# Performance work log

Measured on AMD Instinct MI355X. Metric: run time of the kernel, lower is better.

Reference implementation:

```python
import jax, jax.numpy as jnp
import numpy as np

TRIANGLE_TABLE = np.array([
    [-1, -1, -1, -1, -1, -1], [1, 0, 2, -1, -1, -1], [4, 0, 3, -1, -1, -1], [1, 4, 2, 1, 3, 4],
    [3, 1, 5, -1, -1, -1], [2, 3, 0, 2, 5, 3], [1, 4, 0, 1, 5, 4], [4, 2, 5, -1, -1, -1],
    [4, 5, 2, -1, -1, -1], [4, 1, 0, 4, 5, 1], [3, 2, 0, 3, 5, 2], [1, 3, 5, -1, -1, -1],
    [4, 1, 2, 4, 3, 1], [3, 0, 4, -1, -1, -1], [2, 0, 1, -1, -1, -1], [-1, -1, -1, -1, -1, -1]], np.int32)
NUM_TRIANGLES_TABLE = np.array([0, 1, 1, 2, 1, 2, 2, 1, 1, 2, 2, 1, 2, 1, 1, 0], np.int32)
BASE_TET_EDGES = np.array([0, 1, 0, 2, 0, 3, 1, 2, 1, 3, 2, 3], np.int32)


def _make_tet_grid(R):
    # Regular grid in [0,1]^3, each cube split into 6 tets along the 0-7 diagonal.
    r1 = R + 1
    gi, gj, gk = np.meshgrid(np.arange(r1), np.arange(r1), np.arange(r1), indexing='ij')
    verts = (np.stack([gi, gj, gk], -1).reshape(-1, 3) / R).astype(np.float32)  # (Nv,3)
    ci, cj, ck = np.meshgrid(np.arange(R), np.arange(R), np.arange(R), indexing='ij')
    ci, cj, ck = ci.ravel(), cj.ravel(), ck.ravel()
    def vid(dx, dy, dz):
        return ((ci + dx) * r1 + (cj + dy)) * r1 + (ck + dz)
    corners = [vid((c >> 2) & 1, (c >> 1) & 1, c & 1) for c in range(8)]
    tet_corners = [(0, 1, 3, 7), (0, 3, 2, 7), (0, 2, 6, 7), (0, 6, 4, 7), (0, 4, 5, 7), (0, 5, 1, 7)]
    tets = np.stack([np.stack([corners[a] for a in t], -1) for t in tet_corners], 1).reshape(-1, 4)
    return verts, tets.astype(np.int32)


def setup_inputs() -> dict:
    R = 64
    verts, tets = _make_tet_grid(R)
    key = jax.random.key(0)
    k1, k2 = jax.random.split(key)
    level = jax.random.normal(k1, (verts.shape[0],), dtype=jnp.float32)
    deformation = jax.random.normal(k2, (verts.shape[0], 3), dtype=jnp.float32)
    return {
        'level': level,
        'deformation': deformation,
        'grid_vertices': jnp.asarray(verts),
        'tet_indices': jnp.asarray(tets),
        'resolution': R,
    }


def reference(level, deformation, grid_vertices, tet_indices, resolution):
    # normalize_grid_deformation: (range_hi - range_lo)/res * tanh(offsets), range = (0,1)
    pos = grid_vertices + jnp.tanh(deformation) / resolution  # (Nv,3)
    occ = level > 0                                           # (Nv,)
    occ_f = occ[tet_indices]                                  # (F,4)
    occ_sum = occ_f.sum(-1)
    valid = (occ_sum > 0) & (occ_sum < 4)
    vt = tet_indices[valid]                                   # (Fv,4)
    occ_valid = occ_f[valid]                                  # (Fv,4)
    # per-tet edges, each sorted (min,max) -> dedup
    edges = vt[:, jnp.asarray(BASE_TET_EDGES)].reshape(-1, 2)  # (6*Fv,2)
    edges = jnp.sort(edges, axis=1)
    unique_edges, idx_map = jnp.unique(edges, axis=0, return_inverse=True)
    idx_map = idx_map.reshape(-1)
    # edges that actually cross the isosurface (exactly one endpoint inside)
    mask_edges = occ[unique_edges].sum(-1) == 1               # (U,)
    mapping = jnp.where(mask_edges, jnp.cumsum(mask_edges.astype(jnp.int32)) - 1, -1)
    idx_map = mapping[idx_map].reshape(-1, 6)                 # (Fv,6)
    interp_v = unique_edges[mask_edges]                       # (M,2)
    # linear interpolation of crossing point along each edge
    ep = pos[interp_v]                                        # (M,2,3)
    es = level[interp_v] * jnp.array([1.0, -1.0], dtype=level.dtype)  # (M,2) = [sdf0, -sdf1]
    w = es[:, ::-1] / es.sum(1, keepdims=True)                # (M,2) = [-sdf1, sdf0]/(sdf0-sdf1)
    verts_out = (ep * w[:, :, None]).sum(1)                   # (M,3)
    # triangle table lookup
    v_id = jnp.array([1, 2, 4, 8], dtype=jnp.int32)
    tetindex = (occ_valid.astype(jnp.int32) * v_id).sum(-1)   # (Fv,)
    tri_tab = jnp.asarray(TRIANGLE_TABLE)
    num_tri = jnp.asarray(NUM_TRIANGLES_TABLE)[tetindex]
    m1 = num_tri == 1
    m2 = num_tri == 2
    f1 = jnp.take_along_axis(idx_map[m1], tri_tab[tetindex[m1]][:, :3], axis=1).reshape(-1, 3)
    f2 = jnp.take_along_axis(idx_map[m2], tri_tab[tetindex[m2]][:, :6], axis=1).reshape(-1, 3)
    faces = jnp.concatenate([f1, f2], axis=0)                 # (Nf,3)
    return verts_out, faces
```

## Files before the change

### kernel.cpp

```cpp
#include <hip/hip_runtime.h>
#include <math.h>


typedef unsigned long long ull;

#define ST_LD(p)    __hip_atomic_load((p), __ATOMIC_RELAXED, __HIP_MEMORY_SCOPE_AGENT)
#define ST_ST(p,v)  __hip_atomic_store((p), (v), __ATOMIC_RELAXED, __HIP_MEMORY_SCOPE_AGENT)

__device__ __forceinline__ float fast_tanh(float x) {
    float e = __expf(2.0f * x);
    return __fdividef(e - 1.0f, e + 1.0f);
}

__device__ __forceinline__ int divq(unsigned v, ull M) {
    return (int)(((ull)v * M) >> 46);
}

constexpr int TT[16][6] = {
    {-1,-1,-1,-1,-1,-1},{1,0,2,-1,-1,-1},{4,0,3,-1,-1,-1},{1,4,2,1,3,4},
    {3,1,5,-1,-1,-1},{2,3,0,2,5,3},{1,4,0,1,5,4},{4,2,5,-1,-1,-1},
    {4,5,2,-1,-1,-1},{4,1,0,4,5,1},{3,2,0,3,5,2},{1,3,5,-1,-1,-1},
    {4,1,2,4,3,1},{3,0,4,-1,-1,-1},{2,0,1,-1,-1,-1},{-1,-1,-1,-1,-1,-1}};
constexpr int NTRI[16] = {0,1,1,2,1,2,2,1,1,2,2,1,2,1,1,0};
constexpr int TC[6][4] = {{0,1,3,7},{0,3,2,7},{0,2,6,7},{0,6,4,7},{0,4,5,7},{0,5,1,7}};
constexpr int TE[6][6] = {
    {(0<<3)|0,(0<<3)|2,(0<<3)|6,(1<<3)|1,(1<<3)|5,(3<<3)|3},
    {(0<<3)|2,(0<<3)|1,(0<<3)|6,(2<<3)|0,(3<<3)|3,(2<<3)|4},
    {(0<<3)|1,(0<<3)|5,(0<<3)|6,(2<<3)|3,(2<<3)|4,(6<<3)|0},
    {(0<<3)|5,(0<<3)|3,(0<<3)|6,(4<<3)|1,(6<<3)|0,(4<<3)|2},
    {(0<<3)|3,(0<<3)|4,(0<<3)|6,(4<<3)|0,(4<<3)|2,(5<<3)|1},
    {(0<<3)|4,(0<<3)|0,(0<<3)|6,(1<<3)|3,(5<<3)|1,(1<<3)|5}};

struct DTabT { ull w[2048]; };
constexpr DTabT make_dtab() {
    DTabT t{};
    for (int ob = 0; ob < 256; ob++) {
        for (int k = 0; k < 8; k++) {
            ull w = 0;
            if (k < 6) {
                int ti = ((ob >> TC[k][0]) & 1) | (((ob >> TC[k][1]) & 1) << 1)
                       | (((ob >> TC[k][2]) & 1) << 2) | (((ob >> TC[k][3]) & 1) << 3);
                int nt = NTRI[ti];
                int pre1 = 0, pre2 = 0;
                for (int kk = 0; kk < k; kk++) {
                    int tik = ((ob >> TC[kk][0]) & 1) | (((ob >> TC[kk][1]) & 1) << 1)
                            | (((ob >> TC[kk][2]) & 1) << 2) | (((ob >> TC[kk][3]) & 1) << 3);
                    pre1 += (NTRI[tik] == 1); pre2 += (NTRI[tik] == 2);
                }
                w = (ull)nt | ((ull)pre1 << 2) | ((ull)pre2 << 5);
                for (int e = 0; e < 6; e++) {
                    int le = TT[ti][e];
                    int ce = (le >= 0) ? TE[k][le] : 0;
                    w |= (ull)ce << (8 + 6 * e);
                }
            }
            t.w[ob * 8 + k] = w;
        }
    }
    return t;
}
__device__ __constant__ DTabT c_dtab = make_dtab();

#define TAG      (1ull << 62)
#define PMASK    ((1ull << 60) - 1ull)
#define READY(s) (((s) >> 62) == 1ull)

__global__ void k_vert(const float* __restrict__ level, const float* __restrict__ deform,
                       int NV, int r1, float invR, ull Mrsq, ull Mr1,
                       ull* __restrict__ stateA,
                       unsigned* __restrict__ rankWord, ull* __restrict__ cubeInfo,
                       int* __restrict__ totals, float* __restrict__ out) {
    int b = blockIdx.x;
    int v = b * 256 + threadIdx.x;
    int R = r1 - 1, rsq = r1 * r1;
    bool valid = v < NV;
    float la = valid ? level[v] : 0.f;
    bool occv = valid && (la > 0.f);

    int x = 0, y = 0, z = 0, flags = 0, n1 = 0, n2 = 0, cidx = 0, ob = 0;
    bool interior = false;
    float lb[7];
    if (valid) {
        x = divq((unsigned)v, Mrsq); int rem = v - x * rsq;
        y = divq((unsigned)rem, Mr1); z = rem - y * r1;
        bool bx = x < R, by = y < R, bz = z < R;
        interior = bx && by && bz;
        bool inb[7] = {bz, by, by && bz, bx, bx && bz, bx && by, interior};
        int deltas[7] = {1, r1, r1 + 1, rsq, rsq + 1, rsq + r1, rsq + r1 + 1};
        ob = occv ? 1 : 0;
        #pragma unroll
        for (int j = 0; j < 7; j++) {
            float l = inb[j] ? level[v + deltas[j]] : 0.f;
            lb[j] = l;
            bool o = inb[j] && (l > 0.f);
            ob |= (o ? 1 : 0) << (j + 1);
            if (inb[j] && (o != occv)) flags |= 1 << j;
        }
        if (interior) {
            cidx = ((x * R) + y) * R + z;
            #pragma unroll
            for (int k = 0; k < 6; k++) {
                int ti = ((ob >> TC[k][0]) & 1) | (((ob >> TC[k][1]) & 1) << 1)
                       | (((ob >> TC[k][2]) & 1) << 2) | (((ob >> TC[k][3]) & 1) << 3);
                int p = __popc(ti);
                n1 += (p == 1) || (p == 3);
                n2 += (p == 2);
            }
        }
    }
    int cnt = __popc(flags);
    int pk = n1 | (n2 << 16);
    int lane = threadIdx.x & 63, wv = threadIdx.x >> 6;
    int inclE = cnt, inclT = pk;
    #pragma unroll
    for (int o = 1; o < 64; o <<= 1) {
        int tE = __shfl_up(inclE, o);
        int tT = __shfl_up(inclT, o);
        if (lane >= o) { inclE += tE; inclT += tT; }
    }
    __shared__ int wE[4], wT[4];
    __shared__ ull sPart[4];
    if (lane == 63) { wE[wv] = inclE; wT[wv] = inclT; }
    __syncthreads();

    if (threadIdx.x == 0) {
        int eb = wE[0] + wE[1] + wE[2] + wE[3];
        int tb = wT[0] + wT[1] + wT[2] + wT[3];
        ST_ST(&stateA[b], TAG | ((ull)eb << 40) | ((ull)(tb & 0xffff) << 20) | (ull)(tb >> 16));
    }
    int woffE = 0, woffT = 0;
    for (int w2 = 0; w2 < wv; w2++) { woffE += wE[w2]; woffT += wT[w2]; }
    int localRank = woffE + inclE - cnt;
    int tExcl = woffT + inclT - pk;

    __shared__ float ldsV[5376];
    if (flags) {
        int deltas[7] = {1, r1, r1 + 1, rsq, rsq + 1, rsq + r1, rsq + r1 + 1};
        const int dxs[7] = {0, 0, 0, 1, 1, 1, 1};
        const int dys[7] = {0, 1, 1, 0, 0, 1, 1};
        const int dzs[7] = {1, 0, 1, 0, 1, 0, 1};
        float pax = x * invR + fast_tanh(deform[3 * v])     * invR;
        float pay = y * invR + fast_tanh(deform[3 * v + 1]) * invR;
        float paz = z * invR + fast_tanh(deform[3 * v + 2]) * invR;
        int r = localRank;
        #pragma unroll
        for (int j = 0; j < 7; j++) {
            if ((flags >> j) & 1) {
                int bb = v + deltas[j];
                float lbv = lb[j];
                float inv = __fdividef(1.0f, la - lbv);
                float w0 = -lbv * inv;
                float w1f = la * inv;
                float pbx = (x + dxs[j]) * invR + fast_tanh(deform[3 * bb])     * invR;
                float pby = (y + dys[j]) * invR + fast_tanh(deform[3 * bb + 1]) * invR;
                float pbz = (z + dzs[j]) * invR + fast_tanh(deform[3 * bb + 2]) * invR;
                ldsV[3 * r]     = pax * w0 + pbx * w1f;
                ldsV[3 * r + 1] = pay * w0 + pby * w1f;
                ldsV[3 * r + 2] = paz * w0 + pbz * w1f;
                r++;
            }
        }
    }

    ull psum = 0;
    for (int t = 0;; t++) {
        int base = 64 * (4 * t + wv);
        if (base >= b) break;
        int i = b - 1 - (base + lane);
        ull s = 0;
        if (i >= 0) {
            do { s = ST_LD(&stateA[i]); } while (!READY(s));
            s &= PMASK;
        }
        psum += s;
    }
    #pragma unroll
    for (int o = 1; o < 64; o <<= 1) psum += __shfl_xor(psum, o);
    if (lane == 0) sPart[wv] = psum;
    __syncthreads();

    ull ex = sPart[0] + sPart[1] + sPart[2] + sPart[3];
    int exclE = (int)((ex >> 40) & 0xFFFFF);
    int excl1 = (int)((ex >> 20) & 0xFFFFF);
    int excl2 = (int)(ex & 0xFFFFF);
    int eb2 = wE[0] + wE[1] + wE[2] + wE[3];
    if (threadIdx.x == 0 && b == (int)gridDim.x - 1) {
        int tb = wT[0] + wT[1] + wT[2] + wT[3];
        ull inc = ex + (((ull)eb2 << 40) | ((ull)(tb & 0xffff) << 20) | (ull)(tb >> 16));
        totals[0] = (int)((inc >> 40) & 0xFFFFF);
        totals[1] = (int)((inc >> 20) & 0xFFFFF);
        totals[2] = (int)(inc & 0xFFFFF);
    }
    if (interior)
        cubeInfo[cidx] = (ull)(unsigned)ob
                       | ((ull)(unsigned)(excl1 + (tExcl & 0xffff)) << 8)
                       | ((ull)(unsigned)(excl2 + (tExcl >> 16)) << 28);
    if (valid)
        rankWord[v] = (unsigned)(exclE + localRank) | ((unsigned)flags << 21);

    int tot = 3 * eb2;
    float* dstV = out + 3 * (size_t)exclE;
    for (int i = threadIdx.x; i < tot; i += 256) dstV[i] = ldsV[i];
}

__device__ __forceinline__ unsigned sel8(int c, unsigned r0, unsigned r1_, unsigned r2,
                                         unsigned r3, unsigned r4, unsigned r5,
                                         unsigned r6, unsigned r7) {
    unsigned a01 = (c & 1) ? r1_ : r0;
    unsigned a23 = (c & 1) ? r3 : r2;
    unsigned a45 = (c & 1) ? r5 : r4;
    unsigned a67 = (c & 1) ? r7 : r6;
    unsigned lo = (c & 2) ? a23 : a01;
    unsigned hi = (c & 2) ? a67 : a45;
    return (c & 4) ? hi : lo;
}

__global__ void k_face(int r1, int NC, ull Mrr, ull MR,
                       const ull* __restrict__ cubeInfo,
                       const unsigned* __restrict__ rankWord,
                       const int* __restrict__ totals,
                       float* __restrict__ out) {
    int tid = threadIdx.x;
    int c = blockIdx.x * 256 + tid;
    bool act = c < NC;
    int rsq = r1 * r1, R = r1 - 1, rr = R * R;

    ull info = 0;
    ull w0 = 0, w1 = 0, w2 = 0, w3 = 0, w4 = 0, w5 = 0;
    unsigned rw0=0,rw1=0,rw2=0,rw3=0,rw4=0,rw5=0,rw6=0,rw7=0;
    if (act) {
        info = cubeInfo[c];
        int ob = (int)info & 255;
        const ull* dp = &c_dtab.w[ob << 3];
        ulonglong2 p0 = *reinterpret_cast<const ulonglong2*>(dp);
        ulonglong2 p1 = *reinterpret_cast<const ulonglong2*>(dp + 2);
        ulonglong2 p2 = *reinterpret_cast<const ulonglong2*>(dp + 4);
        w0 = p0.x; w1 = p0.y; w2 = p1.x; w3 = p1.y; w4 = p2.x; w5 = p2.y;
        int cx = divq((unsigned)c, Mrr); int rem = c - cx * rr;
        int cy = divq((unsigned)rem, MR); int cz = rem - cy * R;
        int v = (cx * r1 + cy) * r1 + cz;
        rw0 = rankWord[v];             rw1 = rankWord[v + 1];
        rw2 = rankWord[v + r1];        rw3 = rankWord[v + r1 + 1];
        rw4 = rankWord[v + rsq];       rw5 = rankWord[v + rsq + 1];
        rw6 = rankWord[v + rsq + r1];  rw7 = rankWord[v + rsq + r1 + 1];
    }
    unsigned r1c = (unsigned)((info >> 8) & 0xFFFFF);
    unsigned r2c = (unsigned)((info >> 28) & 0xFFFFF);
    int nt5 = (int)w5 & 3;
    int n1c = (((int)w5 >> 2) & 7) + (nt5 == 1);
    int n2c = (((int)w5 >> 5) & 7) + (nt5 == 2);

    __shared__ unsigned sB1, sB2, sE1, sE2;
    __shared__ float ldsF[9216];
    int lastT = NC - 1 - blockIdx.x * 256; if (lastT > 255) lastT = 255;
    if (tid == 0)     { sB1 = r1c; sB2 = r2c; }
    if (tid == lastT) { sE1 = r1c + (unsigned)n1c; sE2 = r2c + (unsigned)n2c; }
    __syncthreads();

    int n1b = (int)(sE1 - sB1), n2b = (int)(sE2 - sB2);
    float* Lr1 = ldsF;
    float* Lr2 = ldsF + 3 * n1b;

    #define ERANK(ce_)                                                          \
        ({ int ce = (ce_);                                                      \
           unsigned rw = sel8(ce >> 3, rw0,rw1,rw2,rw3,rw4,rw5,rw6,rw7);        \
           (float)((int)(rw & 0x1FFFFF) + __popc((rw >> 21) & ((1u << (ce & 7)) - 1u))); })

    if (act) {
        int local1 = (int)(r1c - sB1);
        int local2 = (int)(r2c - sB2);
        #define DO_TET(wk) do {                                                 \
            int nt = (int)(wk) & 3;                                             \
            if (nt) {                                                           \
                ull we = (wk) >> 8;                                             \
                if (nt == 1) {                                                  \
                    int s = local1 + (((int)(wk) >> 2) & 7);                    \
                    float* d = &Lr1[3 * s];                                     \
                    d[0] = ERANK((int)(we) & 63);                               \
                    d[1] = ERANK((int)(we >> 6) & 63);                          \
                    d[2] = ERANK((int)(we >> 12) & 63);                         \
                } else {                                                        \
                    int s = local2 + (((int)(wk) >> 5) & 7);                    \
                    float* d = &Lr2[6 * s];                                     \
                    d[0] = ERANK((int)(we) & 63);                               \
                    d[1] = ERANK((int)(we >> 6) & 63);                          \
                    d[2] = ERANK((int)(we >> 12) & 63);                         \
                    d[3] = ERANK((int)(we >> 18) & 63);                         \
                    d[4] = ERANK((int)(we >> 24) & 63);                         \
                    d[5] = ERANK((int)(we >> 30) & 63);                         \
                }                                                               \
            }                                                                   \
        } while (0)
        DO_TET(w0); DO_TET(w1); DO_TET(w2); DO_TET(w3); DO_TET(w4); DO_TET(w5);
        #undef DO_TET
    }
    #undef ERANK
    __syncthreads();

    int M = totals[0], N1 = totals[1];
    float* faces = out + 3 * (size_t)M;
    float* d1 = faces + 3 * (size_t)sB1;
    for (int i = tid; i < 3 * n1b; i += 256) d1[i] = ldsF[i];
    float* d2 = faces + 3 * (size_t)N1 + 6 * (size_t)sB2;
    const float* s2 = ldsF + 3 * n1b;
    for (int i = tid; i < 6 * n2b; i += 256) d2[i] = s2[i];
}

extern "C" void kernel_launch(void* const* d_in, const int* in_sizes, int n_in,
                              void* d_out, int out_size, void* d_ws, size_t ws_size,
                              hipStream_t stream) {
    const float* level  = (const float*)d_in[0];
    const float* deform = (const float*)d_in[1];
    int NV = in_sizes[0];
    int r1 = 1;
    while ((long long)r1 * r1 * r1 < (long long)NV) r1++;
    int R = r1 - 1;
    float invR = 1.0f / (float)R;
    int rsq = r1 * r1, rr = R * R;

    ull Mrsq = ((1ull << 46) + (ull)rsq - 1) / (ull)rsq;
    ull Mr1  = ((1ull << 46) + (ull)r1  - 1) / (ull)r1;
    ull Mrr  = ((1ull << 46) + (ull)rr  - 1) / (ull)rr;
    ull MR   = ((1ull << 46) + (ull)R   - 1) / (ull)R;

    int nb = (NV + 255) / 256;
    int NC = R * R * R;
    int nbC = (NC + 255) / 256;

    char* w = (char*)d_ws;
    unsigned* rankWord = (unsigned*)w;
    w += (((size_t)NV * sizeof(unsigned)) + 255) & ~(size_t)255;
    ull* cubeInfo = (ull*)w;
    w += (((size_t)NC * 8) + 255) & ~(size_t)255;
    ull* stateA = (ull*)w;
    w += (((size_t)nb * 8) + 255) & ~(size_t)255;
    int* totals = (int*)w;

    float* out = (float*)d_out;

    k_vert<<<nb, 256, 0, stream>>>(level, deform, NV, r1, invR, Mrsq, Mr1,
                                   stateA, rankWord, cubeInfo, totals, out);
    k_face<<<nbC, 256, 0, stream>>>(r1, NC, Mrr, MR, cubeInfo, rankWord, totals, out);
}
```

Measured before the change: 111.1 us.

## Fuse vertex and face kernels into one launch with per-block ready flags

Merges the vertex-scan kernel and the face-emission kernel into a single kernel. The last nbC blocks also run face generation, after spinning on release/acquire flags from the vertex blocks whose rankWord range they need and on a tagged totals word. This removes the second launch and the global barrier between kernels. In exchange, cross-block spin waits are added, which depend on forward progress of earlier blocks, and the shared LDS buffer becomes larger. Flags are not reset between calls, so a rerun could read stale ready states unless the workspace is cleared.

```diff
diff --git a/kernel.cpp b/kernel.cpp
--- a/kernel.cpp
+++ b/kernel.cpp
@@ -65,14 +65,35 @@
 #define PMASK    ((1ull << 60) - 1ull)
 #define READY(s) (((s) >> 62) == 1ull)
 
-__global__ void k_vert(const float* __restrict__ level, const float* __restrict__ deform,
-                       int NV, int r1, float invR, ull Mrsq, ull Mr1,
-                       ull* __restrict__ stateA,
-                       unsigned* __restrict__ rankWord, ull* __restrict__ cubeInfo,
-                       int* __restrict__ totals, float* __restrict__ out) {
-    int b = blockIdx.x;
-    int v = b * 256 + threadIdx.x;
-    int R = r1 - 1, rsq = r1 * r1;
+__device__ __forceinline__ unsigned sel8(int c, unsigned r0, unsigned r1_, unsigned r2,
+                                         unsigned r3, unsigned r4, unsigned r5,
+                                         unsigned r6, unsigned r7) {
+    unsigned a01 = (c & 1) ? r1_ : r0;
+    unsigned a23 = (c & 1) ? r3 : r2;
+    unsigned a45 = (c & 1) ? r5 : r4;
+    unsigned a67 = (c & 1) ? r7 : r6;
+    unsigned lo = (c & 2) ? a23 : a01;
+    unsigned hi = (c & 2) ? a67 : a45;
+    return (c & 4) ? hi : lo;
+}
+
+__global__ __launch_bounds__(256, 4) void k_all(
+        const float* __restrict__ level, const float* __restrict__ deform,
+        int NV, int NC, int r1, float invR,
+        ull Mrsq, ull Mr1, ull Mrr, ull MR, int FOFF,
+        ull* __restrict__ stateA, ull* __restrict__ flagF, ull* __restrict__ totalsF,
+        unsigned* __restrict__ rankWord, ull* __restrict__ cubeInfo,
+        float* __restrict__ out) {
+    __shared__ float ldsB[9216];
+    __shared__ int wE[4], wT[4];
+    __shared__ ull sPart[4];
+    __shared__ unsigned sB1, sB2, sE1, sE2;
+    __shared__ ull sTot;
+
+    int b = blockIdx.x, tid = threadIdx.x;
+    int v = b * 256 + tid;
+    int R = r1 - 1, rsq = r1 * r1, rr = R * R;
+
     bool valid = v < NV;
     float la = valid ? level[v] : 0.f;
     bool occv = valid && (la > 0.f);
@@ -110,7 +131,7 @@
     }
     int cnt = __popc(flags);
     int pk = n1 | (n2 << 16);
-    int lane = threadIdx.x & 63, wv = threadIdx.x >> 6;
+    int lane = tid & 63, wv = tid >> 6;
     int inclE = cnt, inclT = pk;
     #pragma unroll
     for (int o = 1; o < 64; o <<= 1) {
@@ -118,12 +139,10 @@
         int tT = __shfl_up(inclT, o);
         if (lane >= o) { inclE += tE; inclT += tT; }
     }
-    __shared__ int wE[4], wT[4];
-    __shared__ ull sPart[4];
     if (lane == 63) { wE[wv] = inclE; wT[wv] = inclT; }
     __syncthreads();
 
-    if (threadIdx.x == 0) {
+    if (tid == 0) {
         int eb = wE[0] + wE[1] + wE[2] + wE[3];
         int tb = wT[0] + wT[1] + wT[2] + wT[3];
         ST_ST(&stateA[b], TAG | ((ull)eb << 40) | ((ull)(tb & 0xffff) << 20) | (ull)(tb >> 16));
@@ -133,7 +152,6 @@
     int localRank = woffE + inclE - cnt;
     int tExcl = woffT + inclT - pk;
 
-    __shared__ float ldsV[5376];
     if (flags) {
         int deltas[7] = {1, r1, r1 + 1, rsq, rsq + 1, rsq + r1, rsq + r1 + 1};
         const int dxs[7] = {0, 0, 0, 1, 1, 1, 1};
@@ -154,9 +172,9 @@
                 float pbx = (x + dxs[j]) * invR + fast_tanh(deform[3 * bb])     * invR;
                 float pby = (y + dys[j]) * invR + fast_tanh(deform[3 * bb + 1]) * invR;
                 float pbz = (z + dzs[j]) * invR + fast_tanh(deform[3 * bb + 2]) * invR;
-                ldsV[3 * r]     = pax * w0 + pbx * w1f;
-                ldsV[3 * r + 1] = pay * w0 + pby * w1f;
-                ldsV[3 * r + 2] = paz * w0 + pbz * w1f;
+                ldsB[3 * r]     = pax * w0 + pbx * w1f;
+                ldsB[3 * r + 1] = pay * w0 + pby * w1f;
+                ldsB[3 * r + 2] = paz * w0 + pbz * w1f;
                 r++;
             }
         }
@@ -184,12 +202,10 @@
     int excl1 = (int)((ex >> 20) & 0xFFFFF);
     int excl2 = (int)(ex & 0xFFFFF);
     int eb2 = wE[0] + wE[1] + wE[2] + wE[3];
-    if (threadIdx.x == 0 && b == (int)gridDim.x - 1) {
+    if (tid == 0 && b == (int)gridDim.x - 1) {
         int tb = wT[0] + wT[1] + wT[2] + wT[3];
         ull inc = ex + (((ull)eb2 << 40) | ((ull)(tb & 0xffff) << 20) | (ull)(tb >> 16));
-        totals[0] = (int)((inc >> 40) & 0xFFFFF);
-        totals[1] = (int)((inc >> 20) & 0xFFFFF);
-        totals[2] = (int)(inc & 0xFFFFF);
+        ST_ST(totalsF, TAG | inc);
     }
     if (interior)
         cubeInfo[cidx] = (ull)(unsigned)ob
@@ -198,112 +214,124 @@
     if (valid)
         rankWord[v] = (unsigned)(exclE + localRank) | ((unsigned)flags << 21);
 
-    int tot = 3 * eb2;
-    float* dstV = out + 3 * (size_t)exclE;
-    for (int i = threadIdx.x; i < tot; i += 256) dstV[i] = ldsV[i];
-}
-
-__device__ __forceinline__ unsigned sel8(int c, unsigned r0, unsigned r1_, unsigned r2,
-                                         unsigned r3, unsigned r4, unsigned r5,
-                                         unsigned r6, unsigned r7) {
-    unsigned a01 = (c & 1) ? r1_ : r0;
-    unsigned a23 = (c & 1) ? r3 : r2;
-    unsigned a45 = (c & 1) ? r5 : r4;
-    unsigned a67 = (c & 1) ? r7 : r6;
-    unsigned lo = (c & 2) ? a23 : a01;
-    unsigned hi = (c & 2) ? a67 : a45;
-    return (c & 4) ? hi : lo;
-}
-
-__global__ void k_face(int r1, int NC, ull Mrr, ull MR,
-                       const ull* __restrict__ cubeInfo,
-                       const unsigned* __restrict__ rankWord,
-                       const int* __restrict__ totals,
-                       float* __restrict__ out) {
-    int tid = threadIdx.x;
-    int c = blockIdx.x * 256 + tid;
-    bool act = c < NC;
-    int rsq = r1 * r1, R = r1 - 1, rr = R * R;
-
-    ull info = 0;
-    ull w0 = 0, w1 = 0, w2 = 0, w3 = 0, w4 = 0, w5 = 0;
-    unsigned rw0=0,rw1=0,rw2=0,rw3=0,rw4=0,rw5=0,rw6=0,rw7=0;
-    if (act) {
-        info = cubeInfo[c];
-        int ob = (int)info & 255;
-        const ull* dp = &c_dtab.w[ob << 3];
-        ulonglong2 p0 = *reinterpret_cast<const ulonglong2*>(dp);
-        ulonglong2 p1 = *reinterpret_cast<const ulonglong2*>(dp + 2);
-        ulonglong2 p2 = *reinterpret_cast<const ulonglong2*>(dp + 4);
-        w0 = p0.x; w1 = p0.y; w2 = p1.x; w3 = p1.y; w4 = p2.x; w5 = p2.y;
-        int cx = divq((unsigned)c, Mrr); int rem = c - cx * rr;
-        int cy = divq((unsigned)rem, MR); int cz = rem - cy * R;
-        int v = (cx * r1 + cy) * r1 + cz;
-        rw0 = rankWord[v];             rw1 = rankWord[v + 1];
-        rw2 = rankWord[v + r1];        rw3 = rankWord[v + r1 + 1];
-        rw4 = rankWord[v + rsq];       rw5 = rankWord[v + rsq + 1];
-        rw6 = rankWord[v + rsq + r1];  rw7 = rankWord[v + rsq + r1 + 1];
-    }
-    unsigned r1c = (unsigned)((info >> 8) & 0xFFFFF);
-    unsigned r2c = (unsigned)((info >> 28) & 0xFFFFF);
-    int nt5 = (int)w5 & 3;
-    int n1c = (((int)w5 >> 2) & 7) + (nt5 == 1);
-    int n2c = (((int)w5 >> 5) & 7) + (nt5 == 2);
-
-    __shared__ unsigned sB1, sB2, sE1, sE2;
-    __shared__ float ldsF[9216];
-    int lastT = NC - 1 - blockIdx.x * 256; if (lastT > 255) lastT = 255;
-    if (tid == 0)     { sB1 = r1c; sB2 = r2c; }
-    if (tid == lastT) { sE1 = r1c + (unsigned)n1c; sE2 = r2c + (unsigned)n2c; }
     __syncthreads();
-
-    int n1b = (int)(sE1 - sB1), n2b = (int)(sE2 - sB2);
-    float* Lr1 = ldsF;
-    float* Lr2 = ldsF + 3 * n1b;
-
-    #define ERANK(ce_)                                                          \
-        ({ int ce = (ce_);                                                      \
-           unsigned rw = sel8(ce >> 3, rw0,rw1,rw2,rw3,rw4,rw5,rw6,rw7);        \
-           (float)((int)(rw & 0x1FFFFF) + __popc((rw >> 21) & ((1u << (ce & 7)) - 1u))); })
-
-    if (act) {
-        int local1 = (int)(r1c - sB1);
-        int local2 = (int)(r2c - sB2);
-        #define DO_TET(wk) do {                                                 \
-            int nt = (int)(wk) & 3;                                             \
-            if (nt) {                                                           \
-                ull we = (wk) >> 8;                                             \
-                if (nt == 1) {                                                  \
-                    int s = local1 + (((int)(wk) >> 2) & 7);                    \
-                    float* d = &Lr1[3 * s];                                     \
-                    d[0] = ERANK((int)(we) & 63);                               \
-                    d[1] = ERANK((int)(we >> 6) & 63);                          \
-                    d[2] = ERANK((int)(we >> 12) & 63);                         \
-                } else {                                                        \
-                    int s = local2 + (((int)(wk) >> 5) & 7);                    \
-                    float* d = &Lr2[6 * s];                                     \
-                    d[0] = ERANK((int)(we) & 63);                               \
-                    d[1] = ERANK((int)(we >> 6) & 63);                          \
-                    d[2] = ERANK((int)(we >> 12) & 63);                         \
-                    d[3] = ERANK((int)(we >> 18) & 63);                         \
-                    d[4] = ERANK((int)(we >> 24) & 63);                         \
-                    d[5] = ERANK((int)(we >> 30) & 63);                         \
+    if (tid == 0)
+        __hip_atomic_store(&flagF[b], TAG | 1ull, __ATOMIC_RELEASE, __HIP_MEMORY_SCOPE_AGENT);
+
+    {
+        int tot = 3 * eb2;
+        float* dstV = out + 3 * (size_t)exclE;
+        for (int i = tid; i < tot; i += 256) dstV[i] = ldsB[i];
+    }
+    __syncthreads();
+
+    int fb = b - FOFF;
+    if (fb >= 0) {
+        int c = fb * 256 + tid;
+        bool act = c < NC;
+
+        int c0 = fb * 256;
+        int c1e = c0 + 255; if (c1e > NC - 1) c1e = NC - 1;
+        int cx0 = divq((unsigned)c0, Mrr); int rem0 = c0 - cx0 * rr;
+        int cy0 = divq((unsigned)rem0, MR);
+        int vlo = (cx0 * r1 + cy0) * r1 + (rem0 - cy0 * R);
+        int cx1 = divq((unsigned)c1e, Mrr); int rem1 = c1e - cx1 * rr;
+        int cy1 = divq((unsigned)rem1, MR);
+        int vhi = (cx1 * r1 + cy1) * r1 + (rem1 - cy1 * R) + rsq + r1 + 1;
+        int vbLo = vlo >> 8, vbHi = vhi >> 8;
+        if (tid <= vbHi - vbLo) {
+            ull f;
+            do { f = ST_LD(&flagF[vbLo + tid]); } while (!READY(f));
+        }
+        __syncthreads();
+        __builtin_amdgcn_fence(__ATOMIC_ACQUIRE, "agent");
+
+        ull info = 0;
+        ull w0 = 0, w1 = 0, w2 = 0, w3 = 0, w4 = 0, w5 = 0;
+        unsigned rw0=0,rw1=0,rw2=0,rw3=0,rw4=0,rw5=0,rw6=0,rw7=0;
+        if (act) {
+            info = cubeInfo[c];
+            int obf = (int)info & 255;
+            const ull* dp = &c_dtab.w[obf << 3];
+            ulonglong2 p0 = *reinterpret_cast<const ulonglong2*>(dp);
+            ulonglong2 p1 = *reinterpret_cast<const ulonglong2*>(dp + 2);
+            ulonglong2 p2 = *reinterpret_cast<const ulonglong2*>(dp + 4);
+            w0 = p0.x; w1 = p0.y; w2 = p1.x; w3 = p1.y; w4 = p2.x; w5 = p2.y;
+            int cx = divq((unsigned)c, Mrr); int rem = c - cx * rr;
+            int cy = divq((unsigned)rem, MR); int cz = rem - cy * R;
+            int vc = (cx * r1 + cy) * r1 + cz;
+            rw0 = rankWord[vc];             rw1 = rankWord[vc + 1];
+            rw2 = rankWord[vc + r1];        rw3 = rankWord[vc + r1 + 1];
+            rw4 = rankWord[vc + rsq];       rw5 = rankWord[vc + rsq + 1];
+            rw6 = rankWord[vc + rsq + r1];  rw7 = rankWord[vc + rsq + r1 + 1];
+        }
+        unsigned r1c = (unsigned)((info >> 8) & 0xFFFFF);
+        unsigned r2c = (unsigned)((info >> 28) & 0xFFFFF);
+        int nt5 = (int)w5 & 3;
+        int n1c = (((int)w5 >> 2) & 7) + (nt5 == 1);
+        int n2c = (((int)w5 >> 5) & 7) + (nt5 == 2);
+
+        int lastT = NC - 1 - fb * 256; if (lastT > 255) lastT = 255;
+        if (tid == 0)     { sB1 = r1c; sB2 = r2c; }
+        if (tid == lastT) { sE1 = r1c + (unsigned)n1c; sE2 = r2c + (unsigned)n2c; }
+        __syncthreads();
+
+        int n1b = (int)(sE1 - sB1), n2b = (int)(sE2 - sB2);
+        float* Lr1 = ldsB;
+        float* Lr2 = ldsB + 3 * n1b;
+
+        #define ERANK(ce_)                                                      \
+            ({ int ce = (ce_);                                                  \
+               unsigned rw = sel8(ce >> 3, rw0,rw1,rw2,rw3,rw4,rw5,rw6,rw7);    \
+               (float)((int)(rw & 0x1FFFFF) + __popc((rw >> 21) & ((1u << (ce & 7)) - 1u))); })
+
+        if (act) {
+            int local1 = (int)(r1c - sB1);
+            int local2 = (int)(r2c - sB2);
+            #define DO_TET(wk) do {                                             \
+                int nt = (int)(wk) & 3;                                         \
+                if (nt) {                                                       \
+                    ull we = (wk) >> 8;                                         \
+                    if (nt == 1) {                                              \
+                        int s = local1 + (((int)(wk) >> 2) & 7);                \
+                        float* d = &Lr1[3 * s];                                 \
+                        d[0] = ERANK((int)(we) & 63);                           \
+                        d[1] = ERANK((int)(we >> 6) & 63);                      \
+                        d[2] = ERANK((int)(we >> 12) & 63);                     \
+                    } else {                                                    \
+                        int s = local2 + (((int)(wk) >> 5) & 7);                \
+                        float* d = &Lr2[6 * s];                                 \
+                        d[0] = ERANK((int)(we) & 63);                           \
+                        d[1] = ERANK((int)(we >> 6) & 63);                      \
+                        d[2] = ERANK((int)(we >> 12) & 63);                     \
+                        d[3] = ERANK((int)(we >> 18) & 63);                     \
+                        d[4] = ERANK((int)(we >> 24) & 63);                     \
+                        d[5] = ERANK((int)(we >> 30) & 63);                     \
+                    }                                                           \
                 }                                                               \
-            }                                                                   \
-        } while (0)
-        DO_TET(w0); DO_TET(w1); DO_TET(w2); DO_TET(w3); DO_TET(w4); DO_TET(w5);
-        #undef DO_TET
-    }
-    #undef ERANK
-    __syncthreads();
-
-    int M = totals[0], N1 = totals[1];
-    float* faces = out + 3 * (size_t)M;
-    float* d1 = faces + 3 * (size_t)sB1;
-    for (int i = tid; i < 3 * n1b; i += 256) d1[i] = ldsF[i];
-    float* d2 = faces + 3 * (size_t)N1 + 6 * (size_t)sB2;
-    const float* s2 = ldsF + 3 * n1b;
-    for (int i = tid; i < 6 * n2b; i += 256) d2[i] = s2[i];
+            } while (0)
+            DO_TET(w0); DO_TET(w1); DO_TET(w2); DO_TET(w3); DO_TET(w4); DO_TET(w5);
+            #undef DO_TET
+        }
+        #undef ERANK
+
+        if (tid == 0) {
+            ull t;
+            do { t = ST_LD(totalsF); } while (!READY(t));
+            sTot = t;
+        }
+        __syncthreads();
+
+        ull tot = sTot;
+        int M  = (int)((tot >> 40) & 0xFFFFF);
+        int N1 = (int)((tot >> 20) & 0xFFFFF);
+        float* faces = out + 3 * (size_t)M;
+        float* d1 = faces + 3 * (size_t)sB1;
+        for (int i = tid; i < 3 * n1b; i += 256) d1[i] = ldsB[i];
+        float* d2 = faces + 3 * (size_t)N1 + 6 * (size_t)sB2;
+        const float* s2 = ldsB + 3 * n1b;
+        for (int i = tid; i < 6 * n2b; i += 256) d2[i] = s2[i];
+    }
 }
 
 extern "C" void kernel_launch(void* const* d_in, const int* in_sizes, int n_in,
@@ -326,6 +354,7 @@
     int nb = (NV + 255) / 256;
     int NC = R * R * R;
     int nbC = (NC + 255) / 256;
+    int FOFF = nb - nbC;
 
     char* w = (char*)d_ws;
     unsigned* rankWord = (unsigned*)w;
@@ -334,11 +363,13 @@
     w += (((size_t)NC * 8) + 255) & ~(size_t)255;
     ull* stateA = (ull*)w;
     w += (((size_t)nb * 8) + 255) & ~(size_t)255;
-    int* totals = (int*)w;
+    ull* flagF = (ull*)w;
+    w += (((size_t)nb * 8) + 255) & ~(size_t)255;
+    ull* totalsF = (ull*)w;
 
     float* out = (float*)d_out;
 
-    k_vert<<<nb, 256, 0, stream>>>(level, deform, NV, r1, invR, Mrsq, Mr1,
-                                   stateA, rankWord, cubeInfo, totals, out);
-    k_face<<<nbC, 256, 0, stream>>>(r1, NC, Mrr, MR, cubeInfo, rankWord, totals, out);
-}
+    k_all<<<nb, 256, 0, stream>>>(level, deform, NV, NC, r1, invR,
+                                  Mrsq, Mr1, Mrr, MR, FOFF,
+                                  stateA, flagF, totalsF, rankWord, cubeInfo, out);
+}
```

Result: slower. 163.8 us (+47.4%).
